# Kernel optimization log

Hardware: AMD Instinct MI355X
Metric: run time of the kernel (lower is better)

The kernel has to match this reference:

```python
import jax, jax.numpy as jnp
import numpy as np
from jax import lax

WS = (4, 8, 8)        # window_size (D,H,W)
DIM = 128
HEADS = 4
HD = DIM // HEADS      # 32
SCALE = HD ** -0.5     # swinv1, lif neuron -> head_dim**-0.5
TAU = 2.0
VTH = 1.0
ALPHA = 2.0            # ATan surrogate width


def _rel_pos_index(ws):
    # static numpy computation of relative_position_index, shape (N, N)
    coords = np.stack(np.meshgrid(np.arange(ws[0]), np.arange(ws[1]), np.arange(ws[2]), indexing='ij'))
    cf = coords.reshape(3, -1)                      # (3, N)
    rel = (cf[:, :, None] - cf[:, None, :]).transpose(1, 2, 0).astype(np.int64)  # (N,N,3)
    rel[:, :, 0] += ws[0] - 1
    rel[:, :, 1] += ws[1] - 1
    rel[:, :, 2] += ws[2] - 1
    rel[:, :, 0] *= (2 * ws[1] - 1) * (2 * ws[2] - 1)
    rel[:, :, 1] *= 2 * ws[2] - 1
    return rel.sum(-1)

RPI = _rel_pos_index(WS)  # (N, N) int


@jax.custom_vjp
def spike(x):
    return (x >= 0.0).astype(x.dtype)

def _spike_fwd(x):
    return spike(x), x

def _spike_bwd(x, g):
    # ATan surrogate gradient (spikingjelly default)
    return (g * (ALPHA / (2.0 * (1.0 + (np.pi / 2.0 * ALPHA * x) ** 2))),)

spike.defvjp(_spike_fwd, _spike_bwd)


def lif(x):
    # multi-step LIF over leading time axis: v' = v + (x - v)/tau, hard reset to 0
    def step(v, xt):
        v = v + (xt - v) / TAU
        s = spike(v - VTH)
        return v * (1.0 - s), s
    return lax.scan(step, jnp.zeros_like(x[0]), x)[1]


def setup_inputs() -> dict:
    key = jax.random.key(0)
    ks = jax.random.split(key, 7)
    x = jax.random.normal(ks[0], (WS[0], 256, WS[1], WS[2], DIM), dtype=jnp.float32)
    Wq = jax.random.normal(ks[1], (DIM, DIM), dtype=jnp.float32) * 0.02
    Wk = jax.random.normal(ks[2], (DIM, DIM), dtype=jnp.float32) * 0.02
    Wv = jax.random.normal(ks[3], (DIM, DIM), dtype=jnp.float32) * 0.02
    rpb_table = jax.random.normal(ks[4], ((2 * WS[0] - 1) * (2 * WS[1] - 1) * (2 * WS[2] - 1), HEADS), dtype=jnp.float32) * 0.02
    Wproj = jax.random.normal(ks[5], (DIM, DIM), dtype=jnp.float32) * 0.02
    bproj = jax.random.normal(ks[6], (DIM,), dtype=jnp.float32) * 0.02
    return {"x": x, "Wq": Wq, "Wk": Wk, "Wv": Wv, "rpb_table": rpb_table, "Wproj": Wproj, "bproj": bproj}


def reference(x, Wq, Wk, Wv, rpb_table, Wproj, bproj):
    T, B_, H, W, C = x.shape
    N = T * H * W
    # QKV: linear (no bias) -> spiking neuron over time axis
    q = lif(jnp.einsum('tbhwc,dc->tbhwd', x, Wq))
    k = lif(jnp.einsum('tbhwc,dc->tbhwd', x, Wk))
    v = lif(jnp.einsum('tbhwc,dc->tbhwd', x, Wv))
    # literal row-major reshape as in torch: (T,B_,H,W,C) -> (B_, heads, N, hd)
    q = q.reshape(B_, HEADS, N, HD)
    k = k.reshape(B_, HEADS, N, HD)
    v = v.reshape(B_, HEADS, N, HD)
    # scaled QK^T (NO softmax in the original forward)
    attn = jnp.einsum('bhnd,bhmd->bhnm', q * SCALE, k)
    rpb = rpb_table[RPI.reshape(-1)].reshape(N, N, HEADS).transpose(2, 0, 1)  # (heads,N,N)
    attn = attn + rpb[None]
    out = jnp.einsum('bhnm,bhmd->bhnd', attn, v)
    out = out.reshape(B_, HEADS, T, H, W, HD).transpose(2, 0, 3, 4, 1, 5).reshape(T, B_, H, W, C)
    out = jnp.einsum('tbhwc,dc->tbhwd', out, Wproj) + bproj
    out = lif(out).reshape(B_, N, C)
    return (out, attn)
```

## Files before the change

kernel.cpp:

```cpp
#include <hip/hip_runtime.h>
#include <hip/hip_bf16.h>


typedef __attribute__((ext_vector_type(8))) short bf16x8;
typedef __attribute__((ext_vector_type(4))) float f32x4;

#define MFMA16(a, b, c) __builtin_amdgcn_mfma_f32_16x16x32_bf16((a), (b), (c), 0, 0, 0)

__device__ __forceinline__ unsigned short f2bf(float f) {
    union { __hip_bfloat16 h; unsigned short u; } cv;
    cv.h = __float2bfloat16(f);
    return cv.u;
}

__device__ __forceinline__ void cvt8_store(unsigned short* dst, const float* src) {
    float4 f0 = *(const float4*)(src);
    float4 f1 = *(const float4*)(src + 4);
    unsigned short h[8];
    h[0] = f2bf(f0.x); h[1] = f2bf(f0.y); h[2] = f2bf(f0.z); h[3] = f2bf(f0.w);
    h[4] = f2bf(f1.x); h[5] = f2bf(f1.y); h[6] = f2bf(f1.z); h[7] = f2bf(f1.w);
    *(uint4*)dst = *(const uint4*)h;
}

__global__ __launch_bounds__(256) void k_qkv_lif(
    const float* __restrict__ x,
    const float* __restrict__ Wq,
    const float* __restrict__ Wk,
    const float* __restrict__ Wv,
    const float* __restrict__ tbl,
    unsigned int* __restrict__ qbits,
    unsigned int* __restrict__ kbits,
    unsigned int* __restrict__ vbits,
    float* __restrict__ rpbx)
{
    if (blockIdx.y == 3) {
        int base = blockIdx.x * 1024 + threadIdx.x * 4;
        int hh = base >> 16;
        int n = (base >> 8) & 255, m0 = base & 255;
        int zn = n >> 6, yn = (n >> 3) & 7, xn = n & 7;
        float4 o;
#pragma unroll
        for (int i = 0; i < 4; ++i) {
            int m = m0 + i;
            int zm = m >> 6, ym = (m >> 3) & 7, xm = m & 7;
            int ri = (zn - zm + 3) * 225 + (yn - ym + 7) * 15 + (xn - xm + 7);
            ((float*)&o)[i] = tbl[ri * 4 + hh];
        }
        *(float4*)&rpbx[base] = o;
        return;
    }

    __shared__ unsigned short Wl[128 * 136];
    __shared__ unsigned short Xl[64 * 136];

    const int tid = threadIdx.x;
    const int wv = tid >> 6, lane = tid & 63;
    const int l15 = lane & 15, lh = lane >> 4;
    const int wsel = blockIdx.y;
    const float* W = (wsel == 0) ? Wq : (wsel == 1) ? Wk : Wv;
    unsigned int* bits = (wsel == 0) ? qbits : (wsel == 1) ? kbits : vbits;
    const int B = blockIdx.x;

    {
#pragma unroll
        for (int i = 0; i < 8; ++i) {
            int e = i * 2048 + tid * 8;
            int r = e >> 7, cc = e & 127;
            cvt8_store(&Wl[r * 136 + cc], W + r * 128 + cc);
        }
    }

    f32x4 vst[8];
#pragma unroll
    for (int nt = 0; nt < 8; ++nt) vst[nt] = (f32x4){0.f, 0.f, 0.f, 0.f};

    for (int t = 0; t < 4; ++t) {
        __syncthreads();
        const float* xg = x + t * 2097152 + B * 8192;
#pragma unroll
        for (int i = 0; i < 4; ++i) {
            int e = i * 2048 + tid * 8;
            int r = e >> 7, cc = e & 127;
            cvt8_store(&Xl[r * 136 + cc], xg + r * 128 + cc);
        }
        __syncthreads();

        f32x4 acc[8];
#pragma unroll
        for (int nt = 0; nt < 8; ++nt) acc[nt] = (f32x4){0.f, 0.f, 0.f, 0.f};
#pragma unroll
        for (int kk = 0; kk < 4; ++kk) {
            bf16x8 a = *(const bf16x8*)&Xl[(wv * 16 + l15) * 136 + kk * 32 + lh * 8];
#pragma unroll
            for (int nt = 0; nt < 8; ++nt) {
                bf16x8 b = *(const bf16x8*)&Wl[(nt * 16 + l15) * 136 + kk * 32 + lh * 8];
                acc[nt] = MFMA16(a, b, acc[nt]);
            }
        }
        unsigned short sp[8][4];
#pragma unroll
        for (int nt = 0; nt < 8; ++nt) {
#pragma unroll
            for (int reg = 0; reg < 4; ++reg) {
                float y = acc[nt][reg];
                float v = vst[nt][reg];
                v = v + (y - v) * 0.5f;
                float s = (v >= 1.0f) ? 1.0f : 0.0f;
                vst[nt][reg] = v * (1.0f - s);
                sp[nt][reg] = (s != 0.0f) ? (unsigned short)1 : (unsigned short)0;
            }
        }
        __syncthreads();
#pragma unroll
        for (int nt = 0; nt < 8; ++nt)
#pragma unroll
            for (int reg = 0; reg < 4; ++reg)
                Xl[(wv * 16 + lh * 4 + reg) * 136 + nt * 16 + l15] = sp[nt][reg];
        __syncthreads();
        {
            const unsigned short* rowp = &Xl[(tid >> 2) * 136 + (tid & 3) * 32];
            unsigned int mask = 0;
#pragma unroll
            for (int j8 = 0; j8 < 4; ++j8) {
                uint4 u = *(const uint4*)(rowp + j8 * 8);
                int base = j8 * 8;
                if (u.x & 0xFFFFu) mask |= 1u << (base + 0);
                if (u.x >> 16)     mask |= 1u << (base + 1);
                if (u.y & 0xFFFFu) mask |= 1u << (base + 2);
                if (u.y >> 16)     mask |= 1u << (base + 3);
                if (u.z & 0xFFFFu) mask |= 1u << (base + 4);
                if (u.z >> 16)     mask |= 1u << (base + 5);
                if (u.w & 0xFFFFu) mask |= 1u << (base + 6);
                if (u.w >> 16)     mask |= 1u << (base + 7);
            }
            bits[(t * 256 + B) * 256 + tid] = mask;
        }
    }
}

__global__ __launch_bounds__(256) void k_attn(
    const unsigned int* __restrict__ qbits,
    const unsigned int* __restrict__ kbits,
    const unsigned int* __restrict__ vbits,
    const float* __restrict__ rpbx,
    float* __restrict__ attn_out,
    unsigned short* __restrict__ o_ws)
{
    __shared__ unsigned int  qb[256];
    __shared__ unsigned short vT[32 * 264];
    __shared__ unsigned short attnL[2][32 * 264];

    const int tid = threadIdx.x;
    const int wv = tid >> 6, lane = tid & 63;
    const int l15 = lane & 15, lh = lane >> 4;
    const int g = blockIdx.x, hh = g & 3;

    qb[tid] = qbits[g * 256 + tid];
    uint4 km = *(const uint4*)&kbits[g * 256 + (tid & 63) * 4];
    {
        unsigned int vb = vbits[g * 256 + tid];
#pragma unroll
        for (int d = 0; d < 32; ++d)
            vT[d * 264 + tid] = ((vb >> d) & 1u) ? (unsigned short)0x3F80
                                                 : (unsigned short)0;
    }
    __syncthreads();

    const float SC = 0.17677669529663687f;
    float* attn_b = attn_out + (size_t)g * 65536;
    const float* rp = rpbx + hh * 65536;
    unsigned short* ob = o_ws + g * 8192;
    const int rg = wv, m0 = (tid & 63) * 4;
    const int rt = wv >> 1, nh = wv & 1;

    for (int c = 0; c < 8; ++c) {
        unsigned short* buf = attnL[c & 1];
#pragma unroll
        for (int j = 0; j < 8; ++j) {
            int n = c * 32 + j * 4 + rg;
            unsigned int qn = qb[n];
            float4 rp4 = *(const float4*)&rp[n * 256 + m0];
            f32x4 av;
            av.x = (float)__popc(qn & km.x) * SC + rp4.x;
            av.y = (float)__popc(qn & km.y) * SC + rp4.y;
            av.z = (float)__popc(qn & km.z) * SC + rp4.z;
            av.w = (float)__popc(qn & km.w) * SC + rp4.w;
            __builtin_nontemporal_store(av, (f32x4*)(attn_b + n * 256 + m0));
            unsigned int p0 = (unsigned int)f2bf(av.x) | ((unsigned int)f2bf(av.y) << 16);
            unsigned int p1 = (unsigned int)f2bf(av.z) | ((unsigned int)f2bf(av.w) << 16);
            uint2 pk; pk.x = p0; pk.y = p1;
            *(uint2*)&buf[(j * 4 + rg) * 264 + m0] = pk;
        }
        __syncthreads();
        f32x4 oc = (f32x4){0.f, 0.f, 0.f, 0.f};
#pragma unroll
        for (int kk = 0; kk < 8; ++kk) {
            bf16x8 a = *(const bf16x8*)&buf[(rt * 16 + l15) * 264 + kk * 32 + lh * 8];
            bf16x8 b = *(const bf16x8*)&vT[(nh * 16 + l15) * 264 + kk * 32 + lh * 8];
            oc = MFMA16(a, b, oc);
        }
#pragma unroll
        for (int reg = 0; reg < 4; ++reg) {
            int n = c * 32 + rt * 16 + lh * 4 + reg;
            ob[n * 32 + nh * 16 + l15] = f2bf(oc[reg]);
        }
    }
}

__global__ __launch_bounds__(256) void k_proj_lif(
    const unsigned short* __restrict__ o_ws,
    const float* __restrict__ Wp,
    const float* __restrict__ bp,
    float* __restrict__ out0)
{
    __shared__ unsigned short Wl[128 * 136];
    __shared__ unsigned short Al[64 * 136];

    const int tid = threadIdx.x;
    const int wv = tid >> 6, lane = tid & 63;
    const int l15 = lane & 15, lh = lane >> 4;
    const int b = blockIdx.x;

    {
#pragma unroll
        for (int i = 0; i < 8; ++i) {
            int e = i * 2048 + tid * 8;
            int r = e >> 7, cc = e & 127;
            cvt8_store(&Wl[r * 136 + cc], Wp + r * 128 + cc);
        }
    }

    float biasf[2];
#pragma unroll
    for (int ntl = 0; ntl < 2; ++ntl)
        biasf[ntl] = bp[(wv * 2 + ntl) * 16 + l15];

    const unsigned short* ob = o_ws + b * 32768;

    for (int c = 0; c < 4; ++c) {
        __syncthreads();
#pragma unroll
        for (int i = 0; i < 4; ++i) {
            int e = i * 2048 + tid * 8;
            int lr2 = e >> 7, cc = e & 127;
            int t2 = lr2 >> 4, rit = lr2 & 15;
            int hhh = cc >> 5, hd = cc & 31;
            int n = t2 * 64 + c * 16 + rit;
            *(uint4*)&Al[lr2 * 136 + cc] =
                *(const uint4*)(ob + (hhh * 256 + n) * 32 + hd);
        }
        __syncthreads();

        f32x4 acc[4][2];
#pragma unroll
        for (int t2 = 0; t2 < 4; ++t2)
#pragma unroll
            for (int ntl = 0; ntl < 2; ++ntl)
                acc[t2][ntl] = (f32x4){0.f, 0.f, 0.f, 0.f};
#pragma unroll
        for (int kk = 0; kk < 4; ++kk) {
            bf16x8 a[4];
#pragma unroll
            for (int t2 = 0; t2 < 4; ++t2)
                a[t2] = *(const bf16x8*)&Al[(t2 * 16 + l15) * 136 + kk * 32 + lh * 8];
#pragma unroll
            for (int ntl = 0; ntl < 2; ++ntl) {
                bf16x8 bb = *(const bf16x8*)&Wl[((wv * 2 + ntl) * 16 + l15) * 136 + kk * 32 + lh * 8];
#pragma unroll
                for (int t2 = 0; t2 < 4; ++t2)
                    acc[t2][ntl] = MFMA16(a[t2], bb, acc[t2][ntl]);
            }
        }
#pragma unroll
        for (int ntl = 0; ntl < 2; ++ntl) {
            int d = (wv * 2 + ntl) * 16 + l15;
#pragma unroll
            for (int reg = 0; reg < 4; ++reg) {
                int hw = c * 16 + lh * 4 + reg;
                float v = 0.f;
#pragma unroll
                for (int t2 = 0; t2 < 4; ++t2) {
                    float y = acc[t2][ntl][reg] + biasf[ntl];
                    v = v + (y - v) * 0.5f;
                    float s = (v >= 1.0f) ? 1.0f : 0.0f;
                    v = v * (1.0f - s);
                    __builtin_nontemporal_store(
                        s, out0 + t2 * 2097152 + b * 8192 + hw * 128 + d);
                }
            }
        }
    }
}

extern "C" void kernel_launch(void* const* d_in, const int* in_sizes, int n_in,
                              void* d_out, int out_size, void* d_ws, size_t ws_size,
                              hipStream_t stream)
{
    const float* x   = (const float*)d_in[0];
    const float* Wq  = (const float*)d_in[1];
    const float* Wk  = (const float*)d_in[2];
    const float* Wv  = (const float*)d_in[3];
    const float* tbl = (const float*)d_in[4];
    const float* Wp  = (const float*)d_in[5];
    const float* bp  = (const float*)d_in[6];

    float* out0 = (float*)d_out;
    float* attn = out0 + 8388608;

    unsigned short* o_ws = (unsigned short*)d_ws;
    unsigned int* qbits = (unsigned int*)(o_ws + 8388608);
    unsigned int* kbits = qbits + 262144;
    unsigned int* vbits = kbits + 262144;
    float* rpbx = (float*)(vbits + 262144);

    k_qkv_lif<<<dim3(256, 4), 256, 0, stream>>>(x, Wq, Wk, Wv, tbl,
                                                qbits, kbits, vbits, rpbx);
    k_attn<<<1024, 256, 0, stream>>>(qbits, kbits, vbits, rpbx, attn, o_ws);
    k_proj_lif<<<256, 256, 0, stream>>>(o_ws, Wp, bp, out0);
}
```

Before: 354.4 us.

## Truncate fp32 to bf16 via byte-perm and process two windows per QKV block

```diff
diff --git a/kernel.cpp b/kernel.cpp
--- a/kernel.cpp
+++ b/kernel.cpp
@@ -7,19 +7,23 @@
 
 #define MFMA16(a, b, c) __builtin_amdgcn_mfma_f32_16x16x32_bf16((a), (b), (c), 0, 0, 0)
 
-__device__ __forceinline__ unsigned short f2bf(float f) {
-    union { __hip_bfloat16 h; unsigned short u; } cv;
-    cv.h = __float2bfloat16(f);
-    return cv.u;
+__device__ __forceinline__ unsigned int pk_trunc(float f0, float f1) {
+    return __builtin_amdgcn_perm(__float_as_uint(f1), __float_as_uint(f0),
+                                 0x07060302u);
+}
+__device__ __forceinline__ unsigned short f2bf_trunc(float f) {
+    return (unsigned short)(__float_as_uint(f) >> 16);
 }
 
 __device__ __forceinline__ void cvt8_store(unsigned short* dst, const float* src) {
-    float4 f0 = *(const float4*)(src);
-    float4 f1 = *(const float4*)(src + 4);
-    unsigned short h[8];
-    h[0] = f2bf(f0.x); h[1] = f2bf(f0.y); h[2] = f2bf(f0.z); h[3] = f2bf(f0.w);
-    h[4] = f2bf(f1.x); h[5] = f2bf(f1.y); h[6] = f2bf(f1.z); h[7] = f2bf(f1.w);
-    *(uint4*)dst = *(const uint4*)h;
+    uint4 a = *(const uint4*)(src);
+    uint4 b = *(const uint4*)(src + 4);
+    uint4 o;
+    o.x = __builtin_amdgcn_perm(a.y, a.x, 0x07060302u);
+    o.y = __builtin_amdgcn_perm(a.w, a.z, 0x07060302u);
+    o.z = __builtin_amdgcn_perm(b.y, b.x, 0x07060302u);
+    o.w = __builtin_amdgcn_perm(b.w, b.z, 0x07060302u);
+    *(uint4*)dst = o;
 }
 
 __global__ __launch_bounds__(256) void k_qkv_lif(
@@ -34,19 +38,20 @@
     float* __restrict__ rpbx)
 {
     if (blockIdx.y == 3) {
-        int base = blockIdx.x * 1024 + threadIdx.x * 4;
+        int base = blockIdx.x * 2048 + threadIdx.x * 8;
         int hh = base >> 16;
         int n = (base >> 8) & 255, m0 = base & 255;
         int zn = n >> 6, yn = (n >> 3) & 7, xn = n & 7;
-        float4 o;
-#pragma unroll
-        for (int i = 0; i < 4; ++i) {
+        float o[8];
+#pragma unroll
+        for (int i = 0; i < 8; ++i) {
             int m = m0 + i;
             int zm = m >> 6, ym = (m >> 3) & 7, xm = m & 7;
             int ri = (zn - zm + 3) * 225 + (yn - ym + 7) * 15 + (xn - xm + 7);
-            ((float*)&o)[i] = tbl[ri * 4 + hh];
-        }
-        *(float4*)&rpbx[base] = o;
+            o[i] = tbl[ri * 4 + hh];
+        }
+        *(float4*)&rpbx[base]     = *(float4*)&o[0];
+        *(float4*)&rpbx[base + 4] = *(float4*)&o[4];
         return;
     }
 
@@ -59,7 +64,6 @@
     const int wsel = blockIdx.y;
     const float* W = (wsel == 0) ? Wq : (wsel == 1) ? Wk : Wv;
     unsigned int* bits = (wsel == 0) ? qbits : (wsel == 1) ? kbits : vbits;
-    const int B = blockIdx.x;
 
     {
 #pragma unroll
@@ -70,70 +74,74 @@
         }
     }
 
-    f32x4 vst[8];
-#pragma unroll
-    for (int nt = 0; nt < 8; ++nt) vst[nt] = (f32x4){0.f, 0.f, 0.f, 0.f};
-
-    for (int t = 0; t < 4; ++t) {
-        __syncthreads();
-        const float* xg = x + t * 2097152 + B * 8192;
-#pragma unroll
-        for (int i = 0; i < 4; ++i) {
-            int e = i * 2048 + tid * 8;
-            int r = e >> 7, cc = e & 127;
-            cvt8_store(&Xl[r * 136 + cc], xg + r * 128 + cc);
-        }
-        __syncthreads();
-
-        f32x4 acc[8];
-#pragma unroll
-        for (int nt = 0; nt < 8; ++nt) acc[nt] = (f32x4){0.f, 0.f, 0.f, 0.f};
-#pragma unroll
-        for (int kk = 0; kk < 4; ++kk) {
-            bf16x8 a = *(const bf16x8*)&Xl[(wv * 16 + l15) * 136 + kk * 32 + lh * 8];
+    for (int bb = 0; bb < 2; ++bb) {
+        const int B = blockIdx.x * 2 + bb;
+
+        f32x4 vst[8];
+#pragma unroll
+        for (int nt = 0; nt < 8; ++nt) vst[nt] = (f32x4){0.f, 0.f, 0.f, 0.f};
+
+        for (int t = 0; t < 4; ++t) {
+            __syncthreads();
+            const float* xg = x + t * 2097152 + B * 8192;
+#pragma unroll
+            for (int i = 0; i < 4; ++i) {
+                int e = i * 2048 + tid * 8;
+                int r = e >> 7, cc = e & 127;
+                cvt8_store(&Xl[r * 136 + cc], xg + r * 128 + cc);
+            }
+            __syncthreads();
+
+            f32x4 acc[8];
+#pragma unroll
+            for (int nt = 0; nt < 8; ++nt) acc[nt] = (f32x4){0.f, 0.f, 0.f, 0.f};
+#pragma unroll
+            for (int kk = 0; kk < 4; ++kk) {
+                bf16x8 a = *(const bf16x8*)&Xl[(wv * 16 + l15) * 136 + kk * 32 + lh * 8];
+#pragma unroll
+                for (int nt = 0; nt < 8; ++nt) {
+                    bf16x8 b = *(const bf16x8*)&Wl[(nt * 16 + l15) * 136 + kk * 32 + lh * 8];
+                    acc[nt] = MFMA16(a, b, acc[nt]);
+                }
+            }
+            unsigned short sp[8][4];
 #pragma unroll
             for (int nt = 0; nt < 8; ++nt) {
-                bf16x8 b = *(const bf16x8*)&Wl[(nt * 16 + l15) * 136 + kk * 32 + lh * 8];
-                acc[nt] = MFMA16(a, b, acc[nt]);
-            }
-        }
-        unsigned short sp[8][4];
-#pragma unroll
-        for (int nt = 0; nt < 8; ++nt) {
-#pragma unroll
-            for (int reg = 0; reg < 4; ++reg) {
-                float y = acc[nt][reg];
-                float v = vst[nt][reg];
-                v = v + (y - v) * 0.5f;
-                float s = (v >= 1.0f) ? 1.0f : 0.0f;
-                vst[nt][reg] = v * (1.0f - s);
-                sp[nt][reg] = (s != 0.0f) ? (unsigned short)1 : (unsigned short)0;
-            }
-        }
-        __syncthreads();
-#pragma unroll
-        for (int nt = 0; nt < 8; ++nt)
-#pragma unroll
-            for (int reg = 0; reg < 4; ++reg)
-                Xl[(wv * 16 + lh * 4 + reg) * 136 + nt * 16 + l15] = sp[nt][reg];
-        __syncthreads();
-        {
-            const unsigned short* rowp = &Xl[(tid >> 2) * 136 + (tid & 3) * 32];
-            unsigned int mask = 0;
-#pragma unroll
-            for (int j8 = 0; j8 < 4; ++j8) {
-                uint4 u = *(const uint4*)(rowp + j8 * 8);
-                int base = j8 * 8;
-                if (u.x & 0xFFFFu) mask |= 1u << (base + 0);
-                if (u.x >> 16)     mask |= 1u << (base + 1);
-                if (u.y & 0xFFFFu) mask |= 1u << (base + 2);
-                if (u.y >> 16)     mask |= 1u << (base + 3);
-                if (u.z & 0xFFFFu) mask |= 1u << (base + 4);
-                if (u.z >> 16)     mask |= 1u << (base + 5);
-                if (u.w & 0xFFFFu) mask |= 1u << (base + 6);
-                if (u.w >> 16)     mask |= 1u << (base + 7);
-            }
-            bits[(t * 256 + B) * 256 + tid] = mask;
+#pragma unroll
+                for (int reg = 0; reg < 4; ++reg) {
+                    float y = acc[nt][reg];
+                    float v = vst[nt][reg];
+                    v = v + (y - v) * 0.5f;
+                    float s = (v >= 1.0f) ? 1.0f : 0.0f;
+                    vst[nt][reg] = v * (1.0f - s);
+                    sp[nt][reg] = (s != 0.0f) ? (unsigned short)1 : (unsigned short)0;
+                }
+            }
+            __syncthreads();
+#pragma unroll
+            for (int nt = 0; nt < 8; ++nt)
+#pragma unroll
+                for (int reg = 0; reg < 4; ++reg)
+                    Xl[(wv * 16 + lh * 4 + reg) * 136 + nt * 16 + l15] = sp[nt][reg];
+            __syncthreads();
+            {
+                const unsigned short* rowp = &Xl[(tid >> 2) * 136 + (tid & 3) * 32];
+                unsigned int mask = 0;
+#pragma unroll
+                for (int j8 = 0; j8 < 4; ++j8) {
+                    uint4 u = *(const uint4*)(rowp + j8 * 8);
+                    int base = j8 * 8;
+                    if (u.x & 0xFFFFu) mask |= 1u << (base + 0);
+                    if (u.x >> 16)     mask |= 1u << (base + 1);
+                    if (u.y & 0xFFFFu) mask |= 1u << (base + 2);
+                    if (u.y >> 16)     mask |= 1u << (base + 3);
+                    if (u.z & 0xFFFFu) mask |= 1u << (base + 4);
+                    if (u.z >> 16)     mask |= 1u << (base + 5);
+                    if (u.w & 0xFFFFu) mask |= 1u << (base + 6);
+                    if (u.w >> 16)     mask |= 1u << (base + 7);
+                }
+                bits[(t * 256 + B) * 256 + tid] = mask;
+            }
         }
     }
 }
@@ -186,9 +194,9 @@
             av.z = (float)__popc(qn & km.z) * SC + rp4.z;
             av.w = (float)__popc(qn & km.w) * SC + rp4.w;
             __builtin_nontemporal_store(av, (f32x4*)(attn_b + n * 256 + m0));
-            unsigned int p0 = (unsigned int)f2bf(av.x) | ((unsigned int)f2bf(av.y) << 16);
-            unsigned int p1 = (unsigned int)f2bf(av.z) | ((unsigned int)f2bf(av.w) << 16);
-            uint2 pk; pk.x = p0; pk.y = p1;
+            uint2 pk;
+            pk.x = pk_trunc(av.x, av.y);
+            pk.y = pk_trunc(av.z, av.w);
             *(uint2*)&buf[(j * 4 + rg) * 264 + m0] = pk;
         }
         __syncthreads();
@@ -202,7 +210,7 @@
 #pragma unroll
         for (int reg = 0; reg < 4; ++reg) {
             int n = c * 32 + rt * 16 + lh * 4 + reg;
-            ob[n * 32 + nh * 16 + l15] = f2bf(oc[reg]);
+            ob[n * 32 + nh * 16 + l15] = f2bf_trunc(oc[reg]);
         }
     }
 }
@@ -313,7 +321,7 @@
     unsigned int* vbits = kbits + 262144;
     float* rpbx = (float*)(vbits + 262144);
 
-    k_qkv_lif<<<dim3(256, 4), 256, 0, stream>>>(x, Wq, Wk, Wv, tbl,
+    k_qkv_lif<<<dim3(128, 4), 256, 0, stream>>>(x, Wq, Wk, Wv, tbl,
                                                 qbits, kbits, vbits, rpbx);
     k_attn<<<1024, 256, 0, stream>>>(qbits, kbits, vbits, rpbx, attn, o_ws);
     k_proj_lif<<<256, 256, 0, stream>>>(o_ws, Wp, bp, out0);
```

Result: no change. 355.8 us (+0.4%).
